# Performance work log

Hardware: AMD Instinct MI355X
Metric: run time of the kernel (lower is better)

The kernel has to match this reference:

```python
import jax, jax.numpy as jnp
import numpy as np
import math

K = 8          # wavelet order (k)
C = 64         # channels (c)
ICH = 512      # ich = c*k
ALPHA = 16     # fourier modes
BATCH, SEQ, NH, NE = 4, 3072, 8, 64   # x: [B, L, H, E], H*E == ICH


def _legendre_filters(k):
    # numpy port of FiSSM/FEDformer get_filter(base='legendre', k): PHI0=PHI1=I
    from numpy.polynomial import legendre as npl, polynomial as npp
    phi_c = np.zeros((k, k)); phi2_c = np.zeros((k, k))
    for ki in range(k):
        e = np.zeros(ki + 1); e[ki] = 1.0
        pc = npl.leg2poly(e)                                  # P_ki power coeffs
        p = npp.Polynomial(pc)(npp.Polynomial([-1.0, 2.0]))
        phi_c[ki, :len(p.coef)] = np.sqrt(2 * ki + 1) * p.coef
        p2 = npp.Polynomial(pc)(npp.Polynomial([-1.0, 4.0]))
        phi2_c[ki, :len(p2.coef)] = np.sqrt(2.0) * np.sqrt(2 * ki + 1) * p2.coef

    def _int_half(prod, upper_half):
        prod = prod.copy(); prod[np.abs(prod) < 1e-8] = 0
        n = np.arange(len(prod))
        w = (1 - np.power(0.5, 1 + n)) if upper_half else np.power(0.5, 1 + n)
        return (prod / (n + 1) * w).sum()

    psi1_c = np.zeros((k, k)); psi2_c = np.zeros((k, k))
    for ki in range(k):
        psi1_c[ki] = phi2_c[ki]
        for i in range(k):
            proj = _int_half(np.convolve(phi2_c[ki, :ki + 1], phi_c[i, :i + 1]), False)
            psi1_c[ki] -= proj * phi_c[i]
            psi2_c[ki] -= proj * phi_c[i]
        for j in range(ki):
            proj = _int_half(np.convolve(phi2_c[ki, :ki + 1], psi1_c[j]), False)
            psi1_c[ki] -= proj * psi1_c[j]
            psi2_c[ki] -= proj * psi2_c[j]
        norm1 = _int_half(np.convolve(psi1_c[ki], psi1_c[ki]), False)
        norm2 = _int_half(np.convolve(psi2_c[ki], psi2_c[ki]), True)
        nrm = np.sqrt(norm1 + norm2)
        psi1_c[ki] /= nrm; psi2_c[ki] /= nrm
        psi1_c[np.abs(psi1_c) < 1e-8] = 0; psi2_c[np.abs(psi2_c) < 1e-8] = 0

    nodes, weights = np.polynomial.legendre.leggauss(k)
    xm = (nodes + 1) / 2; wm = weights / 2     # Gauss-Legendre on [0,1]
    pv = np.polynomial.polynomial.polyval
    phi = lambda i, t: pv(t, phi_c[i])
    psi = lambda i, t: np.where(t <= 0.5, pv(t, psi1_c[i]), pv(t, psi2_c[i]))
    H0 = np.zeros((k, k)); H1 = np.zeros((k, k)); G0 = np.zeros((k, k)); G1 = np.zeros((k, k))
    r2 = 1 / np.sqrt(2)
    for ki in range(k):
        for kp in range(k):
            base = wm * phi(kp, xm)
            H0[ki, kp] = r2 * (base * phi(ki, xm / 2)).sum()
            G0[ki, kp] = r2 * (base * psi(ki, xm / 2)).sum()
            H1[ki, kp] = r2 * (base * phi(ki, (xm + 1) / 2)).sum()
            G1[ki, kp] = r2 * (base * psi(ki, (xm + 1) / 2)).sum()
    for M in (H0, H1, G0, G1):
        M[np.abs(M) < 1e-8] = 0
    ec_s = np.concatenate([H0.T, H1.T], 0).astype(np.float32)   # [2k, k]
    ec_d = np.concatenate([G0.T, G1.T], 0).astype(np.float32)
    rc_e = np.concatenate([H0, G0], 0).astype(np.float32)       # H0r=H0@I etc.
    rc_o = np.concatenate([H1, G1], 0).astype(np.float32)
    return ec_s, ec_d, rc_e, rc_o


def _skft(x, wr, wi):
    # sparseKernelFT2d: FFT-domain conv over the sequence axis, low `modes1` bins
    B, L, c, k = x.shape
    xv = x.reshape(B, L, c * k).transpose(0, 2, 1)     # [B, ck, L]
    xf = jnp.fft.rfft(xv)                              # [B, ck, L//2+1]
    nf = L // 2 + 1
    l = min(wr.shape[-1], nf)
    w = jax.lax.complex(wr[:, :, :l], wi[:, :, :l])
    out = jnp.einsum('bix,iox->box', xf[:, :, :l], w)
    out_ft = jnp.zeros((B, c * k, nf), dtype=out.dtype).at[:, :, :l].set(out)
    y = jnp.fft.irfft(out_ft, n=L)                     # torch default n == L (L even here)
    return y.transpose(0, 2, 1).reshape(B, L, c, k)


def _forward(x, Lk0_w, Lk0_b, Lk1_w, Lk1_b, T0_w, T0_b, Ar, Ai, Br, Bi, Cr, Ci, ec_s, ec_d, rc_e, rc_o):
    B, L, H, E = x.shape
    v = x.reshape(B, L, H * E) @ Lk0_w.T + Lk0_b       # Lk0: ich -> c*k
    v = v.reshape(B, L, C, K)
    # --- MWT_CZ2d (nCZ = 1, level offset self.L = 0) ---
    ns = int(math.floor(math.log2(L)))
    nl = 2 ** int(math.ceil(math.log2(L)))
    v = jnp.concatenate([v, v[:, :nl - L]], axis=1)    # circular-style pad to 2^ceil
    Ud, Us = [], []
    for _ in range(ns):                                # wavelet decompose
        xa = jnp.concatenate([v[:, ::2], v[:, 1::2]], axis=-1)   # [B, N/2, c, 2k]
        d = xa @ ec_d
        v = xa @ ec_s
        Ud.append(_skft(d, Ar, Ai) + _skft(v, Br, Bi))
        Us.append(_skft(d, Cr, Ci))
    v = v @ T0_w.T + T0_b                              # T0 on coarsest scale
    for i in range(ns - 1, -1, -1):                    # evenOdd reconstruct
        v = v + Us[i]
        ve = jnp.concatenate([v, Ud[i]], axis=-1)      # [B, N, c, 2k]
        xe = ve @ rc_e
        xo = ve @ rc_o
        v = jnp.stack([xe, xo], axis=2).reshape(xe.shape[0], 2 * xe.shape[1], C, K)
    v = v[:, :L]
    out = v.reshape(B, L, C * K) @ Lk1_w.T + Lk1_b     # Lk1: c*k -> ich
    return out.reshape(B, L, -1, E)


def setup_inputs():
    key = jax.random.key(0)
    ks = jax.random.split(key, 13)
    ck = C * K
    x = jax.random.normal(ks[0], (BATCH, SEQ, NH, NE), jnp.float32)
    l0 = 1.0 / math.sqrt(ICH)
    l1 = 1.0 / math.sqrt(ck)
    lt = 1.0 / math.sqrt(K)
    scale = 1.0 / (ck * ck)
    u = lambda k_, shp, lo, hi: jax.random.uniform(k_, shp, jnp.float32, lo, hi)
    inp = dict(
        x=x,
        Lk0_w=u(ks[1], (ck, ICH), -l0, l0), Lk0_b=u(ks[2], (ck,), -l0, l0),
        Lk1_w=u(ks[3], (ICH, ck), -l1, l1), Lk1_b=u(ks[4], (ICH,), -l1, l1),
        T0_w=u(ks[5], (K, K), -lt, lt), T0_b=u(ks[6], (K,), -lt, lt),
        Ar=scale * u(ks[7], (ck, ck, ALPHA), 0.0, 1.0), Ai=scale * u(ks[8], (ck, ck, ALPHA), 0.0, 1.0),
        Br=scale * u(ks[9], (ck, ck, ALPHA), 0.0, 1.0), Bi=scale * u(ks[10], (ck, ck, ALPHA), 0.0, 1.0),
        Cr=scale * u(ks[11], (ck, ck, ALPHA), 0.0, 1.0), Ci=scale * u(ks[12], (ck, ck, ALPHA), 0.0, 1.0),
    )
    ec_s, ec_d, rc_e, rc_o = _legendre_filters(K)
    inp.update(ec_s=jnp.asarray(ec_s), ec_d=jnp.asarray(ec_d),
               rc_e=jnp.asarray(rc_e), rc_o=jnp.asarray(rc_o))
    return inp


def reference(x, Lk0_w, Lk0_b, Lk1_w, Lk1_b, T0_w, T0_b, Ar, Ai, Br, Bi, Cr, Ci, ec_s, ec_d, rc_e, rc_o):
    return _forward(x, Lk0_w, Lk0_b, Lk1_w, Lk1_b, T0_w, T0_b,
                    Ar, Ai, Br, Bi, Cr, Ci, ec_s, ec_d, rc_e, rc_o)
```

## Files before the change

kernel.cpp:

```cpp
#include <hip/hip_runtime.h>

#define CKD 512
#define NROWS 44
#define XPLANE 360448

static __device__ __forceinline__ int imin(int a, int b) { return a < b ? a : b; }

typedef short bf16x8 __attribute__((ext_vector_type(8)));
typedef float f32x4 __attribute__((ext_vector_type(4)));
typedef unsigned int uint32;

static __device__ __forceinline__ unsigned int pk2(float a, float b) {
  unsigned int ua = __float_as_uint(a), ub = __float_as_uint(b);
  ua = (ua + 0x7fffu + ((ua >> 16) & 1u)) >> 16;
  ub = (ub + 0x7fffu + ((ub >> 16) & 1u)) >> 16;
  return ua | (ub << 16);
}

static __device__ __forceinline__ uint32 ror16(uint32 q) { return (q >> 16) | (q << 16); }

static __device__ __forceinline__ bf16x8 mk_neghi(uint32 q0, uint32 q1, uint32 q2, uint32 q3) {
  union { uint32 u[4]; bf16x8 h; } t;
  t.u[0] = q0 ^ 0x80000000u; t.u[1] = q1 ^ 0x80000000u;
  t.u[2] = q2 ^ 0x80000000u; t.u[3] = q3 ^ 0x80000000u;
  return t.h;
}
static __device__ __forceinline__ bf16x8 mk_swap(uint32 q0, uint32 q1, uint32 q2, uint32 q3) {
  union { uint32 u[4]; bf16x8 h; } t;
  t.u[0] = ror16(q0); t.u[1] = ror16(q1); t.u[2] = ror16(q2); t.u[3] = ror16(q3);
  return t.h;
}

__global__ __launch_bounds__(256) void k_cvt_x(
    const float* __restrict__ src, unsigned short* __restrict__ dst)
{
  int g = blockIdx.x * 256 + threadIdx.x;
  int row = g >> 6, c8 = (g & 63) << 3;
  int b = row >> 12, t = row & 4095;
  if (t >= 3072) t -= 3072;
  const float* s = src + ((size_t)(b * 3072 + t) << 9) + c8;
  float4 v0 = *(const float4*)s;
  float4 v1 = *(const float4*)(s + 4);
  uint4 o = make_uint4(pk2(v0.x, v0.y), pk2(v0.z, v0.w),
                       pk2(v1.x, v1.y), pk2(v1.z, v1.w));
  *(uint4*)(dst + ((size_t)row << 9) + c8) = o;
}

__global__ __launch_bounds__(256) void k_cvt_gen(
    const float* __restrict__ src, unsigned short* __restrict__ dst)
{
  int g = blockIdx.x * 256 + threadIdx.x;
  const float* s = src + ((size_t)g << 3);
  float4 v0 = *(const float4*)s;
  float4 v1 = *(const float4*)(s + 4);
  uint4 o = make_uint4(pk2(v0.x, v0.y), pk2(v0.z, v0.w),
                       pk2(v1.x, v1.y), pk2(v1.z, v1.w));
  *(uint4*)(dst + ((size_t)g << 3)) = o;
}

__global__ __launch_bounds__(256) void k_cvt_c(
    const float* __restrict__ src, unsigned short* __restrict__ dst)
{
  int g = blockIdx.x * 256 + threadIdx.x;
  int row = g >> 6, c8 = (g & 63) << 3;
  int b = row / 3072, t = row - b * 3072;
  const float* s = src + ((size_t)((b << 12) + t) << 9) + c8;
  float4 v0 = *(const float4*)s;
  float4 v1 = *(const float4*)(s + 4);
  uint4 o = make_uint4(pk2(v0.x, v0.y), pk2(v0.z, v0.w),
                       pk2(v1.x, v1.y), pk2(v1.z, v1.w));
  *(uint4*)(dst + ((size_t)row << 9) + c8) = o;
}

__global__ __launch_bounds__(256) void k_gemm_bf16(
    const unsigned short* __restrict__ A, const unsigned short* __restrict__ W,
    const float* __restrict__ bias, float* __restrict__ Out)
{
  __shared__ unsigned short As[128 * 40];
  __shared__ unsigned short Bs[128 * 40];
  const int tid = threadIdx.x;
  const int row = tid >> 1, half = tid & 1;
  const int bm0 = blockIdx.x << 7, bn0 = blockIdx.y << 7;
  const int wv = tid >> 6, l = tid & 63;
  const int wm0 = (wv & 1) << 6, wn0 = (wv >> 1) << 6;
  const int fr = l & 15, fq = l >> 4;

  const unsigned short* Ap = A + (size_t)(bm0 + row) * CKD + half * 16;
  const unsigned short* Wp = W + (size_t)(bn0 + row) * CKD + half * 16;

  f32x4 acc[4][4];
#pragma unroll
  for (int mt = 0; mt < 4; ++mt)
#pragma unroll
    for (int nt = 0; nt < 4; ++nt) {
      acc[mt][nt][0] = 0.f; acc[mt][nt][1] = 0.f;
      acc[mt][nt][2] = 0.f; acc[mt][nt][3] = 0.f;
    }

  for (int k0 = 0; k0 < CKD; k0 += 32) {
    uint4 av0 = *(const uint4*)(Ap + k0);
    uint4 av1 = *(const uint4*)(Ap + k0 + 8);
    uint4 bv0 = *(const uint4*)(Wp + k0);
    uint4 bv1 = *(const uint4*)(Wp + k0 + 8);
    __syncthreads();
    *(uint4*)&As[row * 40 + half * 16]     = av0;
    *(uint4*)&As[row * 40 + half * 16 + 8] = av1;
    *(uint4*)&Bs[row * 40 + half * 16]     = bv0;
    *(uint4*)&Bs[row * 40 + half * 16 + 8] = bv1;
    __syncthreads();
    bf16x8 af[4], bfr[4];
#pragma unroll
    for (int mt = 0; mt < 4; ++mt)
      af[mt] = *(const bf16x8*)&As[(wm0 + mt * 16 + fr) * 40 + fq * 8];
#pragma unroll
    for (int nt = 0; nt < 4; ++nt)
      bfr[nt] = *(const bf16x8*)&Bs[(wn0 + nt * 16 + fr) * 40 + fq * 8];
#pragma unroll
    for (int mt = 0; mt < 4; ++mt)
#pragma unroll
      for (int nt = 0; nt < 4; ++nt)
        acc[mt][nt] = __builtin_amdgcn_mfma_f32_16x16x32_bf16(
            af[mt], bfr[nt], acc[mt][nt], 0, 0, 0);
  }

#pragma unroll
  for (int nt = 0; nt < 4; ++nt) {
    int col = bn0 + wn0 + nt * 16 + fr;
    float bv = bias[col];
#pragma unroll
    for (int mt = 0; mt < 4; ++mt) {
      int r0 = bm0 + wm0 + mt * 16 + fq * 4;
#pragma unroll
      for (int rg = 0; rg < 4; ++rg)
        Out[(size_t)(r0 + rg) * CKD + col] = acc[mt][nt][rg] + bv;
    }
  }
}

__global__ __launch_bounds__(256) void k_decomp_tree(
    const float* __restrict__ Vin, const float* __restrict__ ec_s,
    const float* __restrict__ ec_d, float* __restrict__ DD,
    float* __restrict__ VD, int j0, int NL, int pin)
{
  __shared__ float Es[128], Ed[128];
  __shared__ float bufA[16 * 512];
  __shared__ float bufB[8 * 512];
  const int tid = threadIdx.x;
  if (tid < 128) Es[tid] = ec_s[tid];
  else Ed[tid - 128] = ec_d[tid - 128];
  const int b = blockIdx.y;
  const int t0 = blockIdx.x << 4;

  const float* src = Vin + ((size_t)b * pin + t0) * CKD;
  for (int q = tid; q < 16 * 128; q += 256) {
    int rr = q >> 7, c4 = (q & 127) << 2;
    *(float4*)&bufA[rr * 512 + c4] = *(const float4*)(src + (size_t)rr * CKD + c4);
  }
  __syncthreads();

  float* rd = bufA;
  float* wr = bufB;
  for (int lv = 0; lv < NL; ++lv) {
    const int j = j0 + lv;
    const int Lout = 4096 >> j;
    const int rows = 8 >> lv;
    const int sb = t0 >> (lv + 1);
    const size_t base = 4ull * (4096 - (4096 >> (j - 1))) * CKD;
    float* Dp = DD + base;
    float* Vp = VD + base;
    for (int task = tid; task < rows * 64; task += 256) {
      int s = task >> 6, c = task & 63;
      const float* r0p = rd + (2 * s) * 512 + (c << 3);
      float a[16];
      float4 v0 = *(const float4*)r0p;
      float4 v1 = *(const float4*)(r0p + 4);
      float4 v2 = *(const float4*)(r0p + 512);
      float4 v3 = *(const float4*)(r0p + 516);
      a[0]=v0.x; a[1]=v0.y; a[2]=v0.z; a[3]=v0.w; a[4]=v1.x; a[5]=v1.y; a[6]=v1.z; a[7]=v1.w;
      a[8]=v2.x; a[9]=v2.y; a[10]=v2.z; a[11]=v2.w; a[12]=v3.x; a[13]=v3.y; a[14]=v3.z; a[15]=v3.w;
      float dv[8] = {}, vv[8] = {};
#pragma unroll
      for (int m = 0; m < 16; ++m)
#pragma unroll
        for (int k = 0; k < 8; ++k) {
          dv[k] += a[m] * Ed[m * 8 + k];
          vv[k] += a[m] * Es[m * 8 + k];
        }
      size_t orow = ((size_t)b * Lout + sb + s) * CKD + (c << 3);
      *(float4*)(Dp + orow)     = make_float4(dv[0], dv[1], dv[2], dv[3]);
      *(float4*)(Dp + orow + 4) = make_float4(dv[4], dv[5], dv[6], dv[7]);
      *(float4*)(Vp + orow)     = make_float4(vv[0], vv[1], vv[2], vv[3]);
      *(float4*)(Vp + orow + 4) = make_float4(vv[4], vv[5], vv[6], vv[7]);
      if (lv + 1 < NL) {
        float* wp = wr + s * 512 + (c << 3);
        *(float4*)wp       = make_float4(vv[0], vv[1], vv[2], vv[3]);
        *(float4*)(wp + 4) = make_float4(vv[4], vv[5], vv[6], vv[7]);
      }
    }
    __syncthreads();
    float* t = rd; rd = wr; wr = t;
  }
}

__global__ __launch_bounds__(256) void k_t0(
    const float* __restrict__ Vin, const float* __restrict__ T0w,
    const float* __restrict__ T0b, float* __restrict__ Out)
{
  int g = blockIdx.x * 256 + threadIdx.x;
  if (g >= 4 * 2 * 64) return;
  int c = g & 63;
  int t = (g >> 6) & 1;
  int b = g >> 7;
  const float* src = Vin + ((size_t)(b * 2 + t)) * CKD + (c << 3);
  float a[8];
  float4 v0 = *(const float4*)src;
  float4 v1 = *(const float4*)(src + 4);
  a[0]=v0.x; a[1]=v0.y; a[2]=v0.z; a[3]=v0.w; a[4]=v1.x; a[5]=v1.y; a[6]=v1.z; a[7]=v1.w;
  float o[8];
#pragma unroll
  for (int ko = 0; ko < 8; ++ko) {
    float sum = T0b[ko];
#pragma unroll
    for (int k = 0; k < 8; ++k) sum += a[k] * T0w[ko * 8 + k];
    o[ko] = sum;
  }
  float* dst = Out + ((size_t)(b * 2 + t)) * CKD + (c << 3);
  *(float4*)dst       = make_float4(o[0], o[1], o[2], o[3]);
  *(float4*)(dst + 4) = make_float4(o[4], o[5], o[6], o[7]);
}

__global__ __launch_bounds__(256) void k_fdft(
    const float* __restrict__ DD, const float* __restrict__ VD,
    float* __restrict__ XDre, float* __restrict__ XDim,
    float* __restrict__ XVre, float* __restrict__ XVim)
{
  __shared__ float2 tw[1024];
  int bx = blockIdx.x, j = 1;
  for (;;) {
    int c = (4096 >> j) >> 6; if (c < 1) c = 1;
    if (bx < c) break;
    bx -= c; ++j;
  }
  const int L = 4096 >> j;
  const int t0 = bx << 6;
  const int tcnt = imin(64, L - t0);
  const int b = blockIdx.y;
  const int z = blockIdx.z;
  const int r = (j - 1) * 4 + b;
  const float* src = (z ? VD : DD) +
      ((size_t)(4 * (4096 - (4096 >> (j - 1))) + b * L)) * CKD;
  float* dre = z ? XVre : XDre;
  float* dim_ = z ? XVim : XDim;

  for (int idx = threadIdx.x; idx < 1024; idx += 256) {
    int ff = idx >> 6, tl = idx & 63;
    int t = t0 + tl;
    int m = (2 * ff * t) & (2 * L - 1);
    float xang = (float)m / (float)L;
    tw[idx] = make_float2(cospif(xang), sinpif(xang));
  }
  __syncthreads();

  float ar[16][2] = {};
  float ai[16][2] = {};
  const float* sp = src + (size_t)t0 * CKD + (threadIdx.x << 1);
  float2 nxt = *(const float2*)sp;
  for (int tl = 0; tl < tcnt; ++tl) {
    float2 xv = nxt;
    if (tl + 1 < tcnt) nxt = *(const float2*)(sp + (size_t)(tl + 1) * CKD);
#pragma unroll
    for (int ff = 0; ff < 16; ++ff) {
      float2 cs = tw[(ff << 6) + tl];
      ar[ff][0] += xv.x * cs.x; ar[ff][1] += xv.y * cs.x;
      ai[ff][0] -= xv.x * cs.y; ai[ff][1] -= xv.y * cs.y;
    }
  }
  const int i0 = threadIdx.x << 1;
#pragma unroll
  for (int ff = 0; ff < 16; ++ff) {
    size_t bidx = ((size_t)ff * NROWS + r) * CKD + i0;
    atomicAdd(&dre[bidx], ar[ff][0]);
    atomicAdd(&dre[bidx + 1], ar[ff][1]);
    atomicAdd(&dim_[bidx], ai[ff][0]);
    atomicAdd(&dim_[bidx + 1], ai[ff][1]);
  }
}

__global__ __launch_bounds__(256) void k_transw6b(
    const float* __restrict__ sAr, const float* __restrict__ sAi,
    const float* __restrict__ sBr, const float* __restrict__ sBi,
    const float* __restrict__ sCr, const float* __restrict__ sCi,
    uint2* __restrict__ W4b, uint32* __restrict__ W2b)
{
  int g = blockIdx.x * 256 + threadIdx.x;
  float ar[16], ai[16], br[16], bi[16], cr[16], ci[16];
  const size_t sb = (size_t)g * 16;
#pragma unroll
  for (int q = 0; q < 4; ++q) {
    float4 t;
    t = *(const float4*)(sAr + sb + q * 4); ar[q*4]=t.x; ar[q*4+1]=t.y; ar[q*4+2]=t.z; ar[q*4+3]=t.w;
    t = *(const float4*)(sAi + sb + q * 4); ai[q*4]=t.x; ai[q*4+1]=t.y; ai[q*4+2]=t.z; ai[q*4+3]=t.w;
    t = *(const float4*)(sBr + sb + q * 4); br[q*4]=t.x; br[q*4+1]=t.y; br[q*4+2]=t.z; br[q*4+3]=t.w;
    t = *(const float4*)(sBi + sb + q * 4); bi[q*4]=t.x; bi[q*4+1]=t.y; bi[q*4+2]=t.z; bi[q*4+3]=t.w;
    t = *(const float4*)(sCr + sb + q * 4); cr[q*4]=t.x; cr[q*4+1]=t.y; cr[q*4+2]=t.z; cr[q*4+3]=t.w;
    t = *(const float4*)(sCi + sb + q * 4); ci[q*4]=t.x; ci[q*4+1]=t.y; ci[q*4+2]=t.z; ci[q*4+3]=t.w;
  }
#pragma unroll
  for (int f = 0; f < 16; ++f) {
    size_t e = ((size_t)f << 18) + g;
    W4b[e] = make_uint2(pk2(ar[f], ai[f]), pk2(br[f], bi[f]));
    W2b[e] = pk2(cr[f], ci[f]);
  }
}

__global__ __launch_bounds__(256) void k_packA(
    const float* __restrict__ XDre, const float* __restrict__ XDim,
    const float* __restrict__ XVre, const float* __restrict__ XVim,
    unsigned short* __restrict__ Aud, unsigned short* __restrict__ Aus)
{
  int g = blockIdx.x * 256 + threadIdx.x;
  int f = g / 6144;
  int rem = g - f * 6144;
  int r = rem >> 7, iq = rem & 127;
  uint4 w0 = make_uint4(0,0,0,0), w1 = w0, wu = w0;
  if (r < NROWS) {
    size_t base = ((size_t)f * NROWS + r) * CKD + (iq << 2);
    float4 dre = *(const float4*)(XDre + base);
    float4 dim_ = *(const float4*)(XDim + base);
    float4 vre = *(const float4*)(XVre + base);
    float4 vim = *(const float4*)(XVim + base);
    w0 = make_uint4(pk2(dre.x, dim_.x), pk2(vre.x, vim.x),
                    pk2(dre.y, dim_.y), pk2(vre.y, vim.y));
    w1 = make_uint4(pk2(dre.z, dim_.z), pk2(vre.z, vim.z),
                    pk2(dre.w, dim_.w), pk2(vre.w, vim.w));
    wu = make_uint4(pk2(dre.x, dim_.x), pk2(dre.y, dim_.y),
                    pk2(dre.z, dim_.z), pk2(dre.w, dim_.w));
  }
  size_t du = ((size_t)f * 48 + r) * 2048 + (iq << 4);
  *(uint4*)(Aud + du)     = w0;
  *(uint4*)(Aud + du + 8) = w1;
  *(uint4*)(Aus + ((size_t)f * 48 + r) * 1024 + (iq << 3)) = wu;
}

__global__ __launch_bounds__(256) void k_mixmm(
    const uint2* __restrict__ W4b, const uint32* __restrict__ W2b,
    const unsigned short* __restrict__ Aud, const unsigned short* __restrict__ Aus,
    float* __restrict__ Part)
{
  __shared__ __attribute__((aligned(16))) uint2 sBud[16 * 130];
  __shared__ __attribute__((aligned(16))) uint32 sBus[16 * 132];
  __shared__ __attribute__((aligned(16))) unsigned short sAud[48 * 72];
  __shared__ __attribute__((aligned(16))) unsigned short sAus[48 * 40];

  const int f = blockIdx.x;
  const int o0 = blockIdx.y << 7;
  const int is = blockIdx.z;
  const int i0 = is << 7;
  const int tid = threadIdx.x;
  const int w = tid >> 6, l = tid & 63;
  const int fr = l & 15, fq = l >> 4;
  const int ow0 = w << 5;

  const uint2* gW4 = W4b + ((size_t)f << 18);
  const uint32* gW2 = W2b + ((size_t)f << 18);
  const unsigned short* gAud = Aud + (size_t)f * 48 * 2048;
  const unsigned short* gAus = Aus + (size_t)f * 48 * 1024;

  f32x4 aUd[3][2][2], aUs[3][2][2];
#pragma unroll
  for (int m = 0; m < 3; ++m)
#pragma unroll
    for (int ot = 0; ot < 2; ++ot)
#pragma unroll
      for (int cp = 0; cp < 2; ++cp) {
        aUd[m][ot][cp][0]=0.f; aUd[m][ot][cp][1]=0.f; aUd[m][ot][cp][2]=0.f; aUd[m][ot][cp][3]=0.f;
        aUs[m][ot][cp][0]=0.f; aUs[m][ot][cp][1]=0.f; aUs[m][ot][cp][2]=0.f; aUs[m][ot][cp][3]=0.f;
      }

  for (int ic = 0; ic < 8; ++ic) {
    const int ig = i0 + (ic << 4);
    __syncthreads();
#pragma unroll
    for (int n = 0; n < 4; ++n) {
      int q = tid + (n << 8);
      int il = q >> 6, op = (q & 63) << 1;
      uint4 v = *(const uint4*)(gW4 + (size_t)(ig + il) * 512 + o0 + op);
      *(uint4*)&sBud[il * 130 + op] = v;
    }
#pragma unroll
    for (int n = 0; n < 2; ++n) {
      int q = tid + (n << 8);
      int il = q >> 5, oq = (q & 31) << 2;
      uint4 v = *(const uint4*)(gW2 + (size_t)(ig + il) * 512 + o0 + oq);
      *(uint4*)&sBus[il * 132 + oq] = v;
    }
    {
      int q = tid;
      int m = q >> 3, k8 = (q & 7) << 3;
      uint4 v = *(const uint4*)(gAud + (size_t)m * 2048 + (is << 9) + (ic << 6) + k8);
      *(uint4*)&sAud[m * 72 + k8] = v;
      q = tid + 256;
      if (q < 384) {
        m = q >> 3; k8 = (q & 7) << 3;
        uint4 v2 = *(const uint4*)(gAud + (size_t)m * 2048 + (is << 9) + (ic << 6) + k8);
        *(uint4*)&sAud[m * 72 + k8] = v2;
      }
    }
    if (tid < 192) {
      int m = tid >> 2, k8 = (tid & 3) << 3;
      uint4 v = *(const uint4*)(gAus + (size_t)m * 1024 + (is << 8) + (ic << 5) + k8);
      *(uint4*)&sAus[m * 40 + k8] = v;
    }
    __syncthreads();

#pragma unroll
    for (int ks = 0; ks < 2; ++ks) {
      bf16x8 af[3];
#pragma unroll
      for (int m = 0; m < 3; ++m)
        af[m] = *(const bf16x8*)&sAud[(m * 16 + fr) * 72 + (ks << 5) + (fq << 3)];
#pragma unroll
      for (int ot = 0; ot < 2; ++ot) {
        int ol = ow0 + (ot << 4) + fr;
        int il = (ks << 3) + (fq << 1);
        uint2 qa = sBud[il * 130 + ol];
        uint2 qb = sBud[(il + 1) * 130 + ol];
        bf16x8 b0 = mk_neghi(qa.x, qa.y, qb.x, qb.y);
        bf16x8 b1 = mk_swap(qa.x, qa.y, qb.x, qb.y);
#pragma unroll
        for (int m = 0; m < 3; ++m) {
          aUd[m][ot][0] = __builtin_amdgcn_mfma_f32_16x16x32_bf16(af[m], b0, aUd[m][ot][0], 0, 0, 0);
          aUd[m][ot][1] = __builtin_amdgcn_mfma_f32_16x16x32_bf16(af[m], b1, aUd[m][ot][1], 0, 0, 0);
        }
      }
    }
    {
      bf16x8 af[3];
#pragma unroll
      for (int m = 0; m < 3; ++m)
        af[m] = *(const bf16x8*)&sAus[(m * 16 + fr) * 40 + (fq << 3)];
#pragma unroll
      for (int ot = 0; ot < 2; ++ot) {
        int ol = ow0 + (ot << 4) + fr;
        int il = fq << 2;
        uint32 q0 = sBus[(il + 0) * 132 + ol];
        uint32 q1 = sBus[(il + 1) * 132 + ol];
        uint32 q2 = sBus[(il + 2) * 132 + ol];
        uint32 q3 = sBus[(il + 3) * 132 + ol];
        bf16x8 b0 = mk_neghi(q0, q1, q2, q3);
        bf16x8 b1 = mk_swap(q0, q1, q2, q3);
#pragma unroll
        for (int m = 0; m < 3; ++m) {
          aUs[m][ot][0] = __builtin_amdgcn_mfma_f32_16x16x32_bf16(af[m], b0, aUs[m][ot][0], 0, 0, 0);
          aUs[m][ot][1] = __builtin_amdgcn_mfma_f32_16x16x32_bf16(af[m], b1, aUs[m][ot][1], 0, 0, 0);
        }
      }
    }
  }

  float* P = Part + (size_t)is * 4 * XPLANE;
#pragma unroll
  for (int m = 0; m < 3; ++m) {
#pragma unroll
    for (int reg = 0; reg < 4; ++reg) {
      int r = m * 16 + (fq << 2) + reg;
      if (r < NROWS) {
        size_t rb = ((size_t)f * NROWS + r) * CKD;
#pragma unroll
        for (int ot = 0; ot < 2; ++ot) {
          int col = o0 + ow0 + (ot << 4) + fr;
          P[0 * XPLANE + rb + col] = aUd[m][ot][0][reg];
          P[1 * XPLANE + rb + col] = aUd[m][ot][1][reg];
          P[2 * XPLANE + rb + col] = aUs[m][ot][0][reg];
          P[3 * XPLANE + rb + col] = aUs[m][ot][1][reg];
        }
      }
    }
  }
}

__global__ __launch_bounds__(256) void k_reduce4(
    const float* __restrict__ Part,
    float* __restrict__ UdFre, float* __restrict__ UdFim,
    float* __restrict__ UsFre, float* __restrict__ UsFim)
{
  int idx = blockIdx.x * 256 + threadIdx.x;
  if (idx >= XPLANE) return;
  float s0 = 0.f, s1 = 0.f, s2 = 0.f, s3 = 0.f;
#pragma unroll
  for (int is = 0; is < 4; ++is) {
    const float* p = Part + (size_t)is * 4 * XPLANE;
    s0 += p[0 * XPLANE + idx];
    s1 += p[1 * XPLANE + idx];
    s2 += p[2 * XPLANE + idx];
    s3 += p[3 * XPLANE + idx];
  }
  UdFre[idx] = s0; UdFim[idx] = s1; UsFre[idx] = s2; UsFim[idx] = s3;
}

__global__ __launch_bounds__(512) void k_mix_fb(
    const float* __restrict__ XDre, const float* __restrict__ XDim,
    const float* __restrict__ XVre, const float* __restrict__ XVim,
    const float* __restrict__ war, const float* __restrict__ wai,
    const float* __restrict__ wbr, const float* __restrict__ wbi,
    const float* __restrict__ wcr, const float* __restrict__ wci,
    float* __restrict__ UdFre, float* __restrict__ UdFim,
    float* __restrict__ UsFre, float* __restrict__ UsFim)
{
  const int f = blockIdx.x;
  const int ot = blockIdx.y;
  const int lane = threadIdx.x & 63;
  const int rg = threadIdx.x >> 6;
  const int rbase = (rg < 4) ? rg * 6 : 24 + (rg - 4) * 5;
  const int rcnt = (rg < 4) ? 6 : 5;
  const int o0 = (ot << 7) + lane;
  __shared__ float4 sx[NROWS * 64];
  float udr[6][2] = {}, udi[6][2] = {}, usr[6][2] = {}, usi[6][2] = {};
  for (int i0 = 0; i0 < 512; i0 += 64) {
    __syncthreads();
    for (int idx = threadIdx.x; idx < NROWS * 64; idx += 512) {
      int r = idx >> 6, il = idx & 63;
      size_t xb = ((size_t)f * NROWS + r) * CKD + i0 + il;
      sx[idx] = make_float4(XDre[xb], XDim[xb], XVre[xb], XVim[xb]);
    }
    __syncthreads();
    for (int ii = 0; ii < 64; ++ii) {
      int i = i0 + ii;
      size_t wo = ((((size_t)i << 9) + o0) << 4) + f;
      float4 wa0 = make_float4(war[wo], wai[wo], wbr[wo], wbi[wo]);
      float2 wc0 = make_float2(wcr[wo], wci[wo]);
      size_t w1 = wo + (64u << 4);
      float4 wa1 = make_float4(war[w1], wai[w1], wbr[w1], wbi[w1]);
      float2 wc1 = make_float2(wcr[w1], wci[w1]);
#pragma unroll
      for (int rr = 0; rr < 6; ++rr) {
        if (rr < rcnt) {
          float4 xv = sx[((rbase + rr) << 6) + ii];
          udr[rr][0] += xv.x * wa0.x - xv.y * wa0.y + xv.z * wa0.z - xv.w * wa0.w;
          udi[rr][0] += xv.x * wa0.y + xv.y * wa0.x + xv.z * wa0.w + xv.w * wa0.z;
          usr[rr][0] += xv.x * wc0.x - xv.y * wc0.y;
          usi[rr][0] += xv.x * wc0.y + xv.y * wc0.x;
          udr[rr][1] += xv.x * wa1.x - xv.y * wa1.y + xv.z * wa1.z - xv.w * wa1.w;
          udi[rr][1] += xv.x * wa1.y + xv.y * wa1.x + xv.z * wa1.w + xv.w * wa1.z;
          usr[rr][1] += xv.x * wc1.x - xv.y * wc1.y;
          usi[rr][1] += xv.x * wc1.y + xv.y * wc1.x;
        }
      }
    }
  }
#pragma unroll
  for (int rr = 0; rr < 6; ++rr) {
    if (rr < rcnt) {
      size_t rb_ = ((size_t)f * NROWS + rbase + rr) * CKD;
      UdFre[rb_ + o0] = udr[rr][0];      UdFre[rb_ + o0 + 64] = udr[rr][1];
      UdFim[rb_ + o0] = udi[rr][0];      UdFim[rb_ + o0 + 64] = udi[rr][1];
      UsFre[rb_ + o0] = usr[rr][0];      UsFre[rb_ + o0 + 64] = usr[rr][1];
      UsFim[rb_ + o0] = usi[rr][0];      UsFim[rb_ + o0 + 64] = usi[rr][1];
    }
  }
}

__global__ __launch_bounds__(256) void k_idft(
    const float* __restrict__ UdFre, const float* __restrict__ UdFim,
    const float* __restrict__ UsFre, const float* __restrict__ UsFim,
    float* __restrict__ UdT, float* __restrict__ UsT)
{
  __shared__ float2 tw[128];
  int bx = blockIdx.x, j = 1;
  for (;;) {
    int c = (4096 >> j) >> 3; if (c < 1) c = 1;
    if (bx < c) break;
    bx -= c; ++j;
  }
  const int L = 4096 >> j;
  const int l = imin(16, (L >> 1) + 1);
  const int t0 = bx << 3;
  const int b = blockIdx.y;
  const int r = (j - 1) * 4 + b;
  if (threadIdx.x < 128) {
    int ff = threadIdx.x >> 3, tl = threadIdx.x & 7;
    int t = t0 + tl;
    int m = (2 * ff * t) & (2 * L - 1);
    float xang = (float)m / (float)L;
    float wgt = (ff == 0 || 2 * ff == L) ? 1.0f : 2.0f;
    float sc = wgt / (float)L;
    tw[threadIdx.x] = make_float2(cospif(xang) * sc, sinpif(xang) * sc);
  }
  __syncthreads();
  const int o = threadIdx.x << 1;
  float2 ud[8], us[8];
#pragma unroll
  for (int tl = 0; tl < 8; ++tl) { ud[tl] = make_float2(0.f, 0.f); us[tl] = make_float2(0.f, 0.f); }
  for (int ff = 0; ff < l; ++ff) {
    size_t bidx = ((size_t)ff * NROWS + r) * CKD + o;
    float2 er = *(const float2*)(UdFre + bidx);
    float2 ei = *(const float2*)(UdFim + bidx);
    float2 sr = *(const float2*)(UsFre + bidx);
    float2 si = *(const float2*)(UsFim + bidx);
#pragma unroll
    for (int tl = 0; tl < 8; ++tl) {
      float2 cs = tw[(ff << 3) + tl];
      ud[tl].x += er.x * cs.x - ei.x * cs.y;
      ud[tl].y += er.y * cs.x - ei.y * cs.y;
      us[tl].x += sr.x * cs.x - si.x * cs.y;
      us[tl].y += sr.y * cs.x - si.y * cs.y;
    }
  }
  int tmax = imin(8, L - t0);
  size_t obase = ((size_t)(4 * (4096 - (4096 >> (j - 1))) + b * L + t0)) * CKD + o;
  for (int tl = 0; tl < tmax; ++tl) {
    *(float2*)(UdT + obase + (size_t)tl * CKD) = ud[tl];
    *(float2*)(UsT + obase + (size_t)tl * CKD) = us[tl];
  }
}

__global__ __launch_bounds__(256) void k_recon_tree(
    const float* __restrict__ Vin, const float* __restrict__ UdT,
    const float* __restrict__ UsT, const float* __restrict__ rc_e,
    const float* __restrict__ rc_o, float* __restrict__ Vout,
    int j0, int NL, int ir, int pin, int pout)
{
  __shared__ float Re[128], Ro[128];
  __shared__ float bufA[16 * 512];
  __shared__ float bufB[16 * 512];
  const int tid = threadIdx.x;
  if (tid < 128) Re[tid] = rc_e[tid];
  else Ro[tid - 128] = rc_o[tid - 128];
  const int b = blockIdx.y;
  const int r0 = blockIdx.x * ir;

  for (int q = tid; q < ir * 128; q += 256) {
    int rr = q >> 7, c4 = (q & 127) << 2;
    *(float4*)&bufA[rr * 512 + c4] =
        *(const float4*)(Vin + ((size_t)b * pin + r0 + rr) * CKD + c4);
  }
  __syncthreads();

  float* rd = bufA;
  float* wr = bufB;
  int rows = ir;
  for (int m = 0; m < NL; ++m) {
    const int j = j0 - m;
    const int Lc = 4096 >> j;
    const size_t ab = 4ull * (4096 - (4096 >> (j - 1))) * CKD;
    const int g0 = r0 << m;
    for (int task = tid; task < rows * 64; task += 256) {
      int s = task >> 6, c = task & 63;
      size_t arow = ab + ((size_t)b * Lc + g0 + s) * CKD + (c << 3);
      const float* vp = rd + s * 512 + (c << 3);
      float a[16];
      {
        float4 t0_ = *(const float4*)vp;
        float4 t1_ = *(const float4*)(vp + 4);
        float4 u0 = *(const float4*)(UsT + arow);
        float4 u1 = *(const float4*)(UsT + arow + 4);
        a[0]=t0_.x+u0.x; a[1]=t0_.y+u0.y; a[2]=t0_.z+u0.z; a[3]=t0_.w+u0.w;
        a[4]=t1_.x+u1.x; a[5]=t1_.y+u1.y; a[6]=t1_.z+u1.z; a[7]=t1_.w+u1.w;
        float4 d0 = *(const float4*)(UdT + arow);
        float4 d1 = *(const float4*)(UdT + arow + 4);
        a[8]=d0.x; a[9]=d0.y; a[10]=d0.z; a[11]=d0.w;
        a[12]=d1.x; a[13]=d1.y; a[14]=d1.z; a[15]=d1.w;
      }
      float xe[8] = {}, xo[8] = {};
#pragma unroll
      for (int mm = 0; mm < 16; ++mm)
#pragma unroll
        for (int k = 0; k < 8; ++k) {
          xe[k] += a[mm] * Re[mm * 8 + k];
          xo[k] += a[mm] * Ro[mm * 8 + k];
        }
      float* we = wr + (2 * s) * 512 + (c << 3);
      *(float4*)we         = make_float4(xe[0], xe[1], xe[2], xe[3]);
      *(float4*)(we + 4)   = make_float4(xe[4], xe[5], xe[6], xe[7]);
      *(float4*)(we + 512) = make_float4(xo[0], xo[1], xo[2], xo[3]);
      *(float4*)(we + 516) = make_float4(xo[4], xo[5], xo[6], xo[7]);
    }
    __syncthreads();
    float* t = rd; rd = wr; wr = t;
    rows <<= 1;
  }

  for (int q = tid; q < rows * 128; q += 256) {
    int rr = q >> 7, c4 = (q & 127) << 2;
    *(float4*)(Vout + ((size_t)b * pout + (r0 << NL) + rr) * CKD + c4) =
        *(const float4*)&rd[rr * 512 + c4];
  }
}

extern "C" void kernel_launch(void* const* d_in, const int* in_sizes, int n_in,
                              void* d_out, int out_size, void* d_ws, size_t ws_size,
                              hipStream_t stream)
{
  const float* x     = (const float*)d_in[0];
  const float* Lk0_w = (const float*)d_in[1];
  const float* Lk0_b = (const float*)d_in[2];
  const float* Lk1_w = (const float*)d_in[3];
  const float* Lk1_b = (const float*)d_in[4];
  const float* T0_w  = (const float*)d_in[5];
  const float* T0_b  = (const float*)d_in[6];
  const float* Ar = (const float*)d_in[7];
  const float* Ai = (const float*)d_in[8];
  const float* Br = (const float*)d_in[9];
  const float* Bi = (const float*)d_in[10];
  const float* Cr = (const float*)d_in[11];
  const float* Ci = (const float*)d_in[12];
  const float* ec_s = (const float*)d_in[13];
  const float* ec_d = (const float*)d_in[14];
  const float* rc_e = (const float*)d_in[15];
  const float* rc_o = (const float*)d_in[16];
  float* out = (float*)d_out;

  float* w = (float*)d_ws;
  float* V0 = w;   w += (size_t)4 * 4096 * 512;
  float* VD = w;   w += (size_t)4 * 4094 * 512;
  float* DD = w;   w += (size_t)4 * 4094 * 512;
  float* RB = w;   w += (size_t)4 * 4096 * 512;
  float* XDre = w; w += XPLANE;
  float* XDim = w; w += XPLANE;
  float* XVre = w; w += XPLANE;
  float* XVim = w; w += XPLANE;
  float* UdFre = w; w += XPLANE;
  float* UdFim = w; w += XPLANE;
  float* UsFre = w; w += XPLANE;
  float* UsFim = w; w += XPLANE;
  float* WT = w;
  float* RA = V0;
  float* SA = V0 + 4096;
  float* SB = V0 + 4096 + 32768;
  float* UdT = DD;
  float* UsT = VD;
  float* Part = RB;

  unsigned short* Xb  = (unsigned short*)RB;
  unsigned short* Cb  = (unsigned short*)DD;
  unsigned short* Wb0 = (unsigned short*)UdFre;
  unsigned short* Wb1 = (unsigned short*)UdFre;

  const size_t BASE_FLOATS = 36421632ull;
  const size_t WT_FLOATS   = 25165824ull;
  if (ws_size < BASE_FLOATS * 4) return;
  const bool use_wt = ws_size >= (BASE_FLOATS + WT_FLOATS) * 4;
  uint2*  W4b = (uint2*)WT;
  uint32* W2b = (uint32*)(WT + 8388608ull);
  unsigned short* AudP = (unsigned short*)(WT + 12582912ull);
  unsigned short* AusP = (unsigned short*)(WT + 13369344ull);

  k_cvt_x<<<dim3(4096), dim3(256), 0, stream>>>(x, Xb);
  k_cvt_gen<<<dim3(128), dim3(256), 0, stream>>>(Lk0_w, Wb0);
  k_gemm_bf16<<<dim3(128, 4), dim3(256), 0, stream>>>(Xb, Wb0, Lk0_b, V0);

  k_decomp_tree<<<dim3(256, 4), dim3(256), 0, stream>>>(
      V0, ec_s, ec_d, DD, VD, 1, 4, 4096);
  k_decomp_tree<<<dim3(16, 4), dim3(256), 0, stream>>>(
      VD + 4ull * 3584 * 512, ec_s, ec_d, DD, VD, 5, 4, 256);
  k_decomp_tree<<<dim3(1, 4), dim3(256), 0, stream>>>(
      VD + 4ull * 4064 * 512, ec_s, ec_d, DD, VD, 9, 3, 16);

  k_t0<<<dim3(2), dim3(256), 0, stream>>>(VD + (size_t)4 * 4092 * 512, T0_w, T0_b, RA);

  hipMemsetAsync(XDre, 0, (size_t)4 * XPLANE * 4, stream);

  if (use_wt)
    k_transw6b<<<dim3(1024), dim3(256), 0, stream>>>(Ar, Ai, Br, Bi, Cr, Ci, W4b, W2b);

  k_fdft<<<dim3(68, 4, 2), dim3(256), 0, stream>>>(DD, VD, XDre, XDim, XVre, XVim);

  if (use_wt) {
    k_packA<<<dim3(384), dim3(256), 0, stream>>>(XDre, XDim, XVre, XVim, AudP, AusP);
    k_mixmm<<<dim3(16, 4, 4), dim3(256), 0, stream>>>(W4b, W2b, AudP, AusP, Part);
    k_reduce4<<<dim3((XPLANE + 255) / 256), dim3(256), 0, stream>>>(
        Part, UdFre, UdFim, UsFre, UsFim);
  } else {
    k_mix_fb<<<dim3(16, 4), dim3(512), 0, stream>>>(
        XDre, XDim, XVre, XVim, Ar, Ai, Br, Bi, Cr, Ci,
        UdFre, UdFim, UsFre, UsFim);
  }

  k_idft<<<dim3(513, 4), dim3(256), 0, stream>>>(UdFre, UdFim, UsFre, UsFim, UdT, UsT);

  k_recon_tree<<<dim3(1, 4), dim3(256), 0, stream>>>(
      RA, UdT, UsT, rc_e, rc_o, SA, 11, 3, 2, 2, 16);
  k_recon_tree<<<dim3(16, 4), dim3(256), 0, stream>>>(
      SA, UdT, UsT, rc_e, rc_o, SB, 8, 4, 1, 16, 256);
  k_recon_tree<<<dim3(256, 4), dim3(256), 0, stream>>>(
      SB, UdT, UsT, rc_e, rc_o, RB, 4, 4, 1, 256, 4096);

  k_cvt_c<<<dim3(3072), dim3(256), 0, stream>>>(RB, Cb);
  k_cvt_gen<<<dim3(128), dim3(256), 0, stream>>>(Lk1_w, Wb1);
  k_gemm_bf16<<<dim3(96, 4), dim3(256), 0, stream>>>(Cb, Wb1, Lk1_b, out);
}
```

Measured before the change: 520.8 us.

## Replace fdft atomics with scratch partials plus deterministic reduction kernel

The forward DFT kernel no longer accumulates per-chunk partial sums into the spectrum with float atomicAdd. Levels with more than 64 samples write their partials to a scratch buffer, a new reduction kernel sums them, and single-chunk levels store directly. This also removes the memset of the spectrum buffers and unrolls the time loop by four with grouped loads to improve latency hiding. The cost is an extra kernel launch and a scratch write-then-read of the partials through global memory.

Result: faster. 477.1 us (-8.4%).

```diff
diff --git a/kernel.cpp b/kernel.cpp
--- a/kernel.cpp
+++ b/kernel.cpp
@@ -231,6 +231,7 @@
 
 __global__ __launch_bounds__(256) void k_fdft(
     const float* __restrict__ DD, const float* __restrict__ VD,
+    float* __restrict__ Scr,
     float* __restrict__ XDre, float* __restrict__ XDim,
     float* __restrict__ XVre, float* __restrict__ XVim)
 {
@@ -244,6 +245,7 @@
   const int L = 4096 >> j;
   const int t0 = bx << 6;
   const int tcnt = imin(64, L - t0);
+  const bool multi = (L > 64);
   const int b = blockIdx.y;
   const int z = blockIdx.z;
   const int r = (j - 1) * 4 + b;
@@ -264,26 +266,102 @@
   float ar[16][2] = {};
   float ai[16][2] = {};
   const float* sp = src + (size_t)t0 * CKD + (threadIdx.x << 1);
-  float2 nxt = *(const float2*)sp;
-  for (int tl = 0; tl < tcnt; ++tl) {
-    float2 xv = nxt;
-    if (tl + 1 < tcnt) nxt = *(const float2*)(sp + (size_t)(tl + 1) * CKD);
+
+  if (tcnt >= 4) {
+    float2 q0 = *(const float2*)(sp + 0 * (size_t)CKD);
+    float2 q1 = *(const float2*)(sp + 1 * (size_t)CKD);
+    float2 q2 = *(const float2*)(sp + 2 * (size_t)CKD);
+    float2 q3 = *(const float2*)(sp + 3 * (size_t)CKD);
+    int tl = 0;
+    for (;;) {
+      float2 x0 = q0, x1 = q1, x2 = q2, x3 = q3;
+      const int nx = tl + 4;
+      if (nx < tcnt) {
+        q0 = *(const float2*)(sp + (size_t)(nx + 0) * CKD);
+        q1 = *(const float2*)(sp + (size_t)(nx + 1) * CKD);
+        q2 = *(const float2*)(sp + (size_t)(nx + 2) * CKD);
+        q3 = *(const float2*)(sp + (size_t)(nx + 3) * CKD);
+      }
+#pragma unroll
+      for (int ff = 0; ff < 16; ++ff) {
+        float2 c0 = tw[(ff << 6) + tl + 0];
+        float2 c1 = tw[(ff << 6) + tl + 1];
+        float2 c2 = tw[(ff << 6) + tl + 2];
+        float2 c3 = tw[(ff << 6) + tl + 3];
+        ar[ff][0] += x0.x * c0.x; ar[ff][1] += x0.y * c0.x;
+        ai[ff][0] -= x0.x * c0.y; ai[ff][1] -= x0.y * c0.y;
+        ar[ff][0] += x1.x * c1.x; ar[ff][1] += x1.y * c1.x;
+        ai[ff][0] -= x1.x * c1.y; ai[ff][1] -= x1.y * c1.y;
+        ar[ff][0] += x2.x * c2.x; ar[ff][1] += x2.y * c2.x;
+        ai[ff][0] -= x2.x * c2.y; ai[ff][1] -= x2.y * c2.y;
+        ar[ff][0] += x3.x * c3.x; ar[ff][1] += x3.y * c3.x;
+        ai[ff][0] -= x3.x * c3.y; ai[ff][1] -= x3.y * c3.y;
+      }
+      tl = nx;
+      if (tl >= tcnt) break;
+    }
+  } else {
+    for (int tl = 0; tl < tcnt; ++tl) {
+      float2 xv = *(const float2*)(sp + (size_t)tl * CKD);
+#pragma unroll
+      for (int ff = 0; ff < 16; ++ff) {
+        float2 cs = tw[(ff << 6) + tl];
+        ar[ff][0] += xv.x * cs.x; ar[ff][1] += xv.y * cs.x;
+        ai[ff][0] -= xv.x * cs.y; ai[ff][1] -= xv.y * cs.y;
+      }
+    }
+  }
+
+  const int i0 = threadIdx.x << 1;
+  if (multi) {
+    const int chunk = 64 - (64 >> (j - 1)) + bx;
+    float* S = Scr + ((size_t)((((chunk << 2) + b) << 1) + z)) * 16384;
 #pragma unroll
     for (int ff = 0; ff < 16; ++ff) {
-      float2 cs = tw[(ff << 6) + tl];
-      ar[ff][0] += xv.x * cs.x; ar[ff][1] += xv.y * cs.x;
-      ai[ff][0] -= xv.x * cs.y; ai[ff][1] -= xv.y * cs.y;
-    }
-  }
-  const int i0 = threadIdx.x << 1;
-#pragma unroll
-  for (int ff = 0; ff < 16; ++ff) {
-    size_t bidx = ((size_t)ff * NROWS + r) * CKD + i0;
-    atomicAdd(&dre[bidx], ar[ff][0]);
-    atomicAdd(&dre[bidx + 1], ar[ff][1]);
-    atomicAdd(&dim_[bidx], ai[ff][0]);
-    atomicAdd(&dim_[bidx + 1], ai[ff][1]);
-  }
+      *(float2*)(S + (ff << 10) + i0)       = make_float2(ar[ff][0], ar[ff][1]);
+      *(float2*)(S + (ff << 10) + 512 + i0) = make_float2(ai[ff][0], ai[ff][1]);
+    }
+  } else {
+#pragma unroll
+    for (int ff = 0; ff < 16; ++ff) {
+      size_t bidx = ((size_t)ff * NROWS + r) * CKD + i0;
+      *(float2*)(dre + bidx)  = make_float2(ar[ff][0], ar[ff][1]);
+      *(float2*)(dim_ + bidx) = make_float2(ai[ff][0], ai[ff][1]);
+    }
+  }
+}
+
+__global__ __launch_bounds__(256) void k_fdft_red(
+    const float* __restrict__ Scr,
+    float* __restrict__ XDre, float* __restrict__ XDim,
+    float* __restrict__ XVre, float* __restrict__ XVim)
+{
+  int g = blockIdx.x * 256 + threadIdx.x;
+  int i = g & 511;
+  int part = (g >> 9) & 1;
+  int ff = (g >> 10) & 15;
+  int z = (g >> 14) & 1;
+  int r = g >> 15;
+  int jidx = r >> 2;
+  int b = r & 3;
+  int c = 32 >> jidx;
+  int cbase = 64 - (64 >> jidx);
+  const float* base = Scr
+      + ((size_t)((((cbase << 2) + b) << 1) + z)) * 16384
+      + (ff << 10) + (part << 9) + i;
+  const size_t STR = 8ull * 16384;
+  float s0 = 0.f, s1 = 0.f, s2 = 0.f, s3 = 0.f;
+  int k = 0;
+  for (; k + 4 <= c; k += 4) {
+    s0 += base[(size_t)(k + 0) * STR];
+    s1 += base[(size_t)(k + 1) * STR];
+    s2 += base[(size_t)(k + 2) * STR];
+    s3 += base[(size_t)(k + 3) * STR];
+  }
+  for (; k < c; ++k) s0 += base[(size_t)k * STR];
+  float s = (s0 + s1) + (s2 + s3);
+  float* dst = part ? (z ? XVim : XDim) : (z ? XVre : XDre);
+  dst[((size_t)ff * NROWS + r) * CKD + i] = s;
 }
 
 __global__ __launch_bounds__(256) void k_transw6b(
@@ -730,6 +808,7 @@
   float* UdT = DD;
   float* UsT = VD;
   float* Part = RB;
+  float* Scr  = RB;
 
   unsigned short* Xb  = (unsigned short*)RB;
   unsigned short* Cb  = (unsigned short*)DD;
@@ -758,12 +837,13 @@
 
   k_t0<<<dim3(2), dim3(256), 0, stream>>>(VD + (size_t)4 * 4092 * 512, T0_w, T0_b, RA);
 
-  hipMemsetAsync(XDre, 0, (size_t)4 * XPLANE * 4, stream);
-
   if (use_wt)
     k_transw6b<<<dim3(1024), dim3(256), 0, stream>>>(Ar, Ai, Br, Bi, Cr, Ci, W4b, W2b);
 
-  k_fdft<<<dim3(68, 4, 2), dim3(256), 0, stream>>>(DD, VD, XDre, XDim, XVre, XVim);
+  k_fdft<<<dim3(68, 4, 2), dim3(256), 0, stream>>>(
+      DD, VD, Scr, XDre, XDim, XVre, XVim);
+  k_fdft_red<<<dim3(2560), dim3(256), 0, stream>>>(
+      Scr, XDre, XDim, XVre, XVim);
 
   if (use_wt) {
     k_packA<<<dim3(384), dim3(256), 0, stream>>>(XDre, XDim, XVre, XVim, AudP, AusP);
```
